# Optimization experiments

Measured on AMD Instinct MI355X. Metric: run time of the kernel, lower is better.

Reference implementation:

```python
import jax, jax.numpy as jnp
import numpy as np

NUM_HEADS_Q = 32
NUM_HEADS_KV = 8
HEAD_DIM = 128
THETA = 500000.0
B = 2
S = 1024


def _precompute_freqs(head_dim, seq_len, theta):
    half = head_dim // 2
    freqs = 1.0 / theta ** (jnp.arange(half, dtype=jnp.float32) / half)
    positions = jnp.arange(seq_len, dtype=jnp.float32)
    angles = positions[:, None] * freqs[None, :]  # (S, half)
    return jnp.cos(angles), jnp.sin(angles)


def _apply_rope(x, cos, sin):
    # x: (B, H, S, D); cos/sin: (S, D//2)
    half = x.shape[-1] // 2
    x1, x2 = x[..., :half], x[..., half:]
    c = cos[None, None]
    s = sin[None, None]
    return jnp.concatenate([x1 * c - x2 * s, x1 * s + x2 * c], axis=-1)


def setup_inputs() -> dict:
    key = jax.random.key(0)
    kq, kk, kv = jax.random.split(key, 3)
    q = jax.random.normal(kq, (B, 1, S, NUM_HEADS_Q * HEAD_DIM), dtype=jnp.float32)
    k = jax.random.normal(kk, (B, 1, S, NUM_HEADS_KV * HEAD_DIM), dtype=jnp.float32)
    v = jax.random.normal(kv, (B, 1, S, NUM_HEADS_KV * HEAD_DIM), dtype=jnp.float32)
    return {"q": q, "k": k, "v": v}


def reference(q, k, v) -> jnp.ndarray:
    D = HEAD_DIM
    gqa = NUM_HEADS_Q // NUM_HEADS_KV
    scale = 1.0 / np.sqrt(D).astype(np.float32)

    # (B,1,S,H*D) -> (B,H,S,D)
    qh = q.reshape(B, S, NUM_HEADS_Q, D).transpose(0, 2, 1, 3)
    kh = k.reshape(B, S, NUM_HEADS_KV, D).transpose(0, 2, 1, 3)
    vh = v.reshape(B, S, NUM_HEADS_KV, D).transpose(0, 2, 1, 3)

    cos, sin = _precompute_freqs(D, S, THETA)
    qh = _apply_rope(qh, cos, sin)
    kh = _apply_rope(kh, cos, sin)

    if gqa > 1:
        kh = jnp.repeat(kh, gqa, axis=1)   # (B, Hq, S, D)
        vh = jnp.repeat(vh, gqa, axis=1)

    scores = jnp.einsum('bhqd,bhkd->bhqk', qh, kh) * scale  # (B, Hq, S, S)
    causal = jnp.tril(jnp.ones((S, S), dtype=bool))
    scores = jnp.where(causal[None, None], scores, -jnp.inf)
    weights = jax.nn.softmax(scores, axis=-1)
    attn = jnp.einsum('bhqk,bhkd->bhqd', weights, vh)  # (B, Hq, S, D)
    out = attn.transpose(0, 2, 1, 3).reshape(B, 1, S, NUM_HEADS_Q * D)
    return out
```

## Files before the change

kernel.cpp:

```cpp
#include <hip/hip_runtime.h>
#include <math.h>

typedef __attribute__((ext_vector_type(4))) float f32x4;
typedef __attribute__((ext_vector_type(16))) float f32x16;
typedef __attribute__((ext_vector_type(8))) short bf16x8;

namespace {
constexpr int kB = 2;
constexpr int kS = 1024;
constexpr int kD = 128;
constexpr float kScale = 0.08838834764831845f;
constexpr float kLog2e = 1.4426950408889634f;
constexpr float kFreqC = 0.20503692777194262f;
constexpr int kKPad = 136;
constexpr int kVPad = 72;

constexpr size_t kTabOff = 0;
constexpr size_t kKOff = 512 * 1024;
constexpr size_t kVOff = kKOff + 4194304;
constexpr size_t kWsNeed = kVOff + 4194304;
}

#define VMCNT(n) asm volatile("s_waitcnt vmcnt(" #n ")" ::: "memory")

__device__ inline short f2bf(float f) {
  union { float f; unsigned u; } c{f};
  unsigned r = c.u + 0x7fffu + ((c.u >> 16) & 1u);
  return (short)(r >> 16);
}

__device__ inline unsigned pkbf(float a, float b) {
  unsigned r;
  asm("v_cvt_pk_bf16_f32 %0, %1, %2" : "=v"(r) : "v"(a), "v"(b));
  return r;
}

__device__ inline void gload16(const void* g, void* l) {
  __builtin_amdgcn_global_load_lds(
      (const __attribute__((address_space(1))) void*)g,
      (__attribute__((address_space(3))) void*)l, 16, 0, 0);
}

__global__ __launch_bounds__(256) void rope_table_k(float2* __restrict__ tab) {
  int t = blockIdx.x * 256 + threadIdx.x;
  int pos = t >> 6, j = t & 63;
  float ang = (float)pos * expf(-(float)j * kFreqC);
  float sn, cs;
  sincosf(ang, &sn, &cs);
  tab[t] = make_float2(cs, sn);
}

__global__ __launch_bounds__(256) void prep_k(
    const float* __restrict__ k, const float* __restrict__ v,
    const float2* __restrict__ tab, short* __restrict__ Kp,
    short* __restrict__ Vp) {
  __shared__ float Tl[64][68];
  int bid = blockIdx.x;
  if (bid < 1024) {
    int t2 = bid * 256 + threadIdx.x;
    int j = (t2 & 15) * 4;
    int h = (t2 >> 4) & 7;
    int s = (t2 >> 7) & 1023;
    int b = t2 >> 17;
    size_t sidx = ((size_t)b * 1024 + s) * 1024 + h * 128 + j;
    size_t didx = (((size_t)b * 8 + h) * 1024 + s) * 128 + j;
    float4 x1 = *(const float4*)&k[sidx];
    float4 x2 = *(const float4*)&k[sidx + 64];
    float4 t0 = *(const float4*)&tab[s * 64 + j];
    float4 t1 = *(const float4*)&tab[s * 64 + j + 2];
    short4 y1, y2;
    y1.x = f2bf(x1.x * t0.x - x2.x * t0.y);
    y2.x = f2bf(x1.x * t0.y + x2.x * t0.x);
    y1.y = f2bf(x1.y * t0.z - x2.y * t0.w);
    y2.y = f2bf(x1.y * t0.w + x2.y * t0.z);
    y1.z = f2bf(x1.z * t1.x - x2.z * t1.y);
    y2.z = f2bf(x1.z * t1.y + x2.z * t1.x);
    y1.w = f2bf(x1.w * t1.z - x2.w * t1.w);
    y2.w = f2bf(x1.w * t1.w + x2.w * t1.z);
    *(short4*)&Kp[didx] = y1;
    *(short4*)&Kp[didx + 64] = y2;
  } else {
    int blk = bid - 1024;
    int bh = blk >> 5;
    int rem = blk & 31;
    int s0 = (rem >> 1) * 64;
    int d0 = (rem & 1) * 64;
    int t = threadIdx.x;
#pragma unroll
    for (int i = 0; i < 4; ++i) {
      int srow = i * 16 + (t >> 4);
      int scol = (t & 15) * 4;
      float4 x = *(const float4*)&v[((size_t)(bh >> 3) * 1024 + s0 + srow) * 1024 +
                                    (bh & 7) * 128 + d0 + scol];
      *(float4*)&Tl[srow][scol] = x;
    }
    __syncthreads();
#pragma unroll
    for (int i = 0; i < 4; ++i) {
      int drow = i * 16 + (t >> 4);
      int sq = (t & 15) * 4;
      short4 y;
      y.x = f2bf(Tl[sq + 0][drow]);
      y.y = f2bf(Tl[sq + 1][drow]);
      y.z = f2bf(Tl[sq + 2][drow]);
      y.w = f2bf(Tl[sq + 3][drow]);
      *(short4*)&Vp[((size_t)bh * 128 + d0 + drow) * 1024 + s0 + sq] = y;
    }
  }
}

__global__ __launch_bounds__(256, 2) void attn32_k(
    const float* __restrict__ q, const short* __restrict__ Kp,
    const short* __restrict__ Vp, const float2* __restrict__ tab,
    float* __restrict__ out) {
  __shared__ char KV[2][32768];

  const int tid = threadIdx.x;
  const int w = tid >> 6;
  const int lane = tid & 63;
  const int l31 = lane & 31;
  const int hi5 = lane >> 5;
  const int f = ((int)blockIdx.x + (int)blockIdx.y) & 7;
  const int b = blockIdx.z;
  const int qt = b ? (7 - f) : f;
  const int hq = blockIdx.y;
  const int hkv = hq >> 2;
  const int q0 = qt * 128;
  const int nk = 2 * (qt + 1);

  const char* Kh = (const char*)(Kp + ((size_t)b * 8 + hkv) * 1024 * 128);
  const char* Vh = (const char*)(Vp + ((size_t)b * 8 + hkv) * 128 * 1024);

#define STAGE(k0_, bufi_)                                                     \
  {                                                                           \
    char* Kd = KV[bufi_];                                                     \
    char* Vd = KV[bufi_] + 16384;                                             \
    _Pragma("unroll") for (int ii = 0; ii < 4; ++ii) {                        \
      int i = w * 4 + ii;                                                     \
      int row = i * 4 + (lane >> 4);                                          \
      int srcb = ((k0_) + row) * 256 + (((lane & 15) * 16) ^ ((row & 7) << 4)); \
      gload16(Kh + srcb, Kd + i * 1024);                                      \
    }                                                                         \
    _Pragma("unroll") for (int ii = 0; ii < 4; ++ii) {                        \
      int i = w * 4 + ii;                                                     \
      int d = i * 8 + (lane >> 3);                                            \
      int srcb = d * 2048 + (k0_) * 2 + (((lane & 7) * 16) ^ ((d & 7) << 4)); \
      gload16(Vh + srcb, Vd + i * 1024);                                      \
    }                                                                         \
  }

  STAGE(0, 0);

  const int qrow = q0 + w * 32 + l31;
  const float* qp = q + ((size_t)b * 1024 + qrow) * 4096 + hq * 128;
  const float2* tp = tab + (size_t)qrow * 64;
  bf16x8 qB[8];
#pragma unroll
  for (int g = 0; g < 4; ++g) {
    int jb = g * 16 + hi5 * 8;
    float4 x1a = *(const float4*)&qp[jb];
    float4 x1b = *(const float4*)&qp[jb + 4];
    float4 x2a = *(const float4*)&qp[jb + 64];
    float4 x2b = *(const float4*)&qp[jb + 68];
    float4 t0 = *(const float4*)&tp[jb];
    float4 t1 = *(const float4*)&tp[jb + 2];
    float4 t2 = *(const float4*)&tp[jb + 4];
    float4 t3 = *(const float4*)&tp[jb + 6];
    float lo[8], hb[8];
    lo[0] = (x1a.x * t0.x - x2a.x * t0.y) * kScale;
    hb[0] = (x1a.x * t0.y + x2a.x * t0.x) * kScale;
    lo[1] = (x1a.y * t0.z - x2a.y * t0.w) * kScale;
    hb[1] = (x1a.y * t0.w + x2a.y * t0.z) * kScale;
    lo[2] = (x1a.z * t1.x - x2a.z * t1.y) * kScale;
    hb[2] = (x1a.z * t1.y + x2a.z * t1.x) * kScale;
    lo[3] = (x1a.w * t1.z - x2a.w * t1.w) * kScale;
    hb[3] = (x1a.w * t1.w + x2a.w * t1.z) * kScale;
    lo[4] = (x1b.x * t2.x - x2b.x * t2.y) * kScale;
    hb[4] = (x1b.x * t2.y + x2b.x * t2.x) * kScale;
    lo[5] = (x1b.y * t2.z - x2b.y * t2.w) * kScale;
    hb[5] = (x1b.y * t2.w + x2b.y * t2.z) * kScale;
    lo[6] = (x1b.z * t3.x - x2b.z * t3.y) * kScale;
    hb[6] = (x1b.z * t3.y + x2b.z * t3.x) * kScale;
    lo[7] = (x1b.w * t3.z - x2b.w * t3.w) * kScale;
    hb[7] = (x1b.w * t3.w + x2b.w * t3.z) * kScale;
    union { unsigned u[4]; bf16x8 v; } A, C;
#pragma unroll
    for (int ww = 0; ww < 4; ++ww) {
      A.u[ww] = pkbf(lo[2 * ww], lo[2 * ww + 1]);
      C.u[ww] = pkbf(hb[2 * ww], hb[2 * ww + 1]);
    }
    qB[g] = A.v;
    qB[g + 4] = C.v;
  }

  float m = -3e38f, l = 0.f;
  f32x16 acc[4];
#pragma unroll
  for (int dt = 0; dt < 4; ++dt)
#pragma unroll
    for (int e = 0; e < 16; ++e) acc[dt][e] = 0.f;

  int buf = 0;
  for (int t = 0; t < nk; ++t) {
    if (t < nk - 1) {
      STAGE((t + 1) * 64, buf ^ 1);
      VMCNT(8);
    } else {
      VMCNT(0);
    }
    __builtin_amdgcn_sched_barrier(0);
    __builtin_amdgcn_s_barrier();
    __builtin_amdgcn_sched_barrier(0);

    const char* Ks = KV[buf];
    const char* Vt = KV[buf] + 16384;

    f32x16 sc0, sc1;
#pragma unroll
    for (int e = 0; e < 16; ++e) { sc0[e] = 0.f; sc1[e] = 0.f; }
    const int kswz = (l31 & 7) << 4;
    __builtin_amdgcn_s_setprio(1);
#pragma unroll
    for (int c = 0; c < 8; ++c) {
      int off = c * 32 + hi5 * 16;
      bf16x8 k0f = *(const bf16x8*)(Ks + l31 * 256 + (off ^ kswz));
      bf16x8 k1f = *(const bf16x8*)(Ks + (32 + l31) * 256 + (off ^ kswz));
      sc0 = __builtin_amdgcn_mfma_f32_32x32x16_bf16(k0f, qB[c], sc0, 0, 0, 0);
      sc1 = __builtin_amdgcn_mfma_f32_32x32x16_bf16(k1f, qB[c], sc1, 0, 0, 0);
    }
    __builtin_amdgcn_s_setprio(0);

    if (64 * (t + 1) > q0 + 32 * w) {
      int kb = t * 64 + hi5 * 4;
#pragma unroll
      for (int r = 0; r < 16; ++r) {
        int off = (r & 3) + 8 * (r >> 2);
        if (kb + off > qrow) sc0[r] = -3e38f;
        if (kb + 32 + off > qrow) sc1[r] = -3e38f;
      }
    }

    float tv = -3e38f;
#pragma unroll
    for (int r = 0; r < 16; ++r) tv = fmaxf(tv, fmaxf(sc0[r], sc1[r]));
    tv = fmaxf(tv, __shfl_xor(tv, 32));
    if (!__all(tv <= m + 8.f)) {
      float mn = fmaxf(m, tv);
      float al = exp2f((m - mn) * kLog2e);
      m = mn;
      l *= al;
#pragma unroll
      for (int r = 0; r < 16; ++r) {
        float alr = __shfl(al, (r & 3) + 8 * (r >> 2) + 4 * hi5);
        acc[0][r] *= alr;
        acc[1][r] *= alr;
        acc[2][r] *= alr;
        acc[3][r] *= alr;
      }
    }
    float rs = 0.f;
#pragma unroll
    for (int r = 0; r < 16; ++r) {
      sc0[r] = exp2f((sc0[r] - m) * kLog2e);
      sc1[r] = exp2f((sc1[r] - m) * kLog2e);
      rs += sc0[r] + sc1[r];
    }
    rs += __shfl_xor(rs, 32);
    l += rs;

    __builtin_amdgcn_s_setprio(1);
#define PV_CHUNK(S, CI)                                                       \
    {                                                                         \
      unsigned p0 = pkbf(S[8 * ((CI) & 1) + 0], S[8 * ((CI) & 1) + 1]);       \
      unsigned p1 = pkbf(S[8 * ((CI) & 1) + 2], S[8 * ((CI) & 1) + 3]);       \
      unsigned p2 = pkbf(S[8 * ((CI) & 1) + 4], S[8 * ((CI) & 1) + 5]);       \
      unsigned p3 = pkbf(S[8 * ((CI) & 1) + 6], S[8 * ((CI) & 1) + 7]);       \
      asm("v_permlane32_swap_b32 %0, %1" : "+v"(p0), "+v"(p2));               \
      asm("v_permlane32_swap_b32 %0, %1" : "+v"(p1), "+v"(p3));               \
      union { unsigned u[4]; bf16x8 v; } pa;                                  \
      pa.u[0] = p0; pa.u[1] = p1; pa.u[2] = p2; pa.u[3] = p3;                 \
      int ko = (CI) * 32 + hi5 * 16;                                          \
      _Pragma("unroll") for (int dt = 0; dt < 4; ++dt) {                      \
        int d = dt * 32 + l31;                                                \
        bf16x8 vf = *(const bf16x8*)(Vt + d * 128 + (ko ^ ((d & 7) << 4)));   \
        acc[dt] =                                                             \
            __builtin_amdgcn_mfma_f32_32x32x16_bf16(pa.v, vf, acc[dt], 0, 0, 0); \
      }                                                                       \
    }
    PV_CHUNK(sc0, 0)
    PV_CHUNK(sc0, 1)
    PV_CHUNK(sc1, 2)
    PV_CHUNK(sc1, 3)
#undef PV_CHUNK
    __builtin_amdgcn_s_setprio(0);

    __builtin_amdgcn_sched_barrier(0);
    __builtin_amdgcn_s_barrier();
    __builtin_amdgcn_sched_barrier(0);
    buf ^= 1;
  }

  float linv = 1.f / l;
  const size_t obase = ((size_t)b * 1024 + q0 + w * 32) * 4096 + (size_t)hq * 128;
#pragma unroll
  for (int r = 0; r < 16; ++r) {
    int rq = (r & 3) + 8 * (r >> 2) + 4 * hi5;
    float ilr = __shfl(linv, rq);
    float* orow = out + obase + (size_t)rq * 4096 + l31;
    orow[0]  = acc[0][r] * ilr;
    orow[32] = acc[1][r] * ilr;
    orow[64] = acc[2][r] * ilr;
    orow[96] = acc[3][r] * ilr;
  }
#undef STAGE
}

template <bool USE_TAB>
__global__ __launch_bounds__(256) void attn_k(
    const float* __restrict__ q, const float* __restrict__ k,
    const float* __restrict__ v, const float2* __restrict__ tab,
    float* __restrict__ out) {
  __shared__ short Ksf[64][kKPad];
  __shared__ short Vtf[kD][kVPad];
  __shared__ short Qbuf[64 * kKPad];
  const int tid = threadIdx.x;
  const int w = tid >> 6;
  const int lane = tid & 63;
  const int lrow = lane & 15;
  const int lk8 = (lane >> 4) * 8;
  const int qt = (int)gridDim.x - 1 - (int)blockIdx.x;
  const int hq = blockIdx.y;
  const int b = blockIdx.z;
  const int hkv = hq >> 2;
  const int q0 = qt * 64;
  const float* qb = q + (size_t)b * kS * 4096 + hq * kD;
  const float* kb = k + (size_t)b * kS * 1024 + hkv * kD;
  const float* vb = v + (size_t)b * kS * 1024 + hkv * kD;
#pragma unroll
  for (int it = 0; it < 16; ++it) {
    int pi = tid + it * 256;
    int row = pi >> 6, j = pi & 63;
    int pos = q0 + row;
    float x1 = qb[(size_t)pos * 4096 + j];
    float x2 = qb[(size_t)pos * 4096 + j + 64];
    float c, s;
    if (USE_TAB) { float2 t2 = tab[(pos << 6) + j]; c = t2.x; s = t2.y; }
    else { float ang = (float)pos * __expf(-(float)j * kFreqC); __sincosf(ang, &s, &c); }
    Qbuf[row * kKPad + j]      = f2bf((x1 * c - x2 * s) * kScale);
    Qbuf[row * kKPad + j + 64] = f2bf((x1 * s + x2 * c) * kScale);
  }
  __syncthreads();
  bf16x8 qf[4];
#pragma unroll
  for (int d = 0; d < 4; ++d)
    qf[d] = *(const bf16x8*)&Qbuf[(w * 16 + lrow) * kKPad + d * 32 + lk8];
  __syncthreads();
  short* myP = Qbuf + w * 16 * kVPad;
  float mS[4] = {-3e38f, -3e38f, -3e38f, -3e38f};
  float lS[4] = {0.f, 0.f, 0.f, 0.f};
  f32x4 acc[8];
#pragma unroll
  for (int dt = 0; dt < 8; ++dt) acc[dt] = f32x4{0.f, 0.f, 0.f, 0.f};
  for (int kt = 0; kt <= qt; ++kt) {
    const int k0 = kt * 64;
#pragma unroll
    for (int it = 0; it < 16; ++it) {
      int pi = tid + it * 256;
      int row = pi >> 6, j = pi & 63;
      int pos = k0 + row;
      float x1 = kb[(size_t)pos * 1024 + j];
      float x2 = kb[(size_t)pos * 1024 + j + 64];
      float c, s;
      if (USE_TAB) { float2 t2 = tab[(pos << 6) + j]; c = t2.x; s = t2.y; }
      else { float ang = (float)pos * __expf(-(float)j * kFreqC); __sincosf(ang, &s, &c); }
      Ksf[row][j]      = f2bf(x1 * c - x2 * s);
      Ksf[row][j + 64] = f2bf(x1 * s + x2 * c);
    }
#pragma unroll
    for (int it = 0; it < 8; ++it) {
      int f = (tid + it * 256) * 4;
      int row = f >> 7, col = f & 127;
      const float4 v4 = *(const float4*)(vb + (size_t)(k0 + row) * 1024 + col);
      Vtf[col + 0][row] = f2bf(v4.x);
      Vtf[col + 1][row] = f2bf(v4.y);
      Vtf[col + 2][row] = f2bf(v4.z);
      Vtf[col + 3][row] = f2bf(v4.w);
    }
    __syncthreads();
    f32x4 sc[4];
#pragma unroll
    for (int ct = 0; ct < 4; ++ct) {
      sc[ct] = f32x4{0.f, 0.f, 0.f, 0.f};
#pragma unroll
      for (int d = 0; d < 4; ++d) {
        bf16x8 kf = *(const bf16x8*)&Ksf[ct * 16 + lrow][d * 32 + lk8];
        sc[ct] = __builtin_amdgcn_mfma_f32_16x16x32_bf16(qf[d], kf, sc[ct], 0, 0, 0);
      }
    }
    if (kt == qt) {
#pragma unroll
      for (int ct = 0; ct < 4; ++ct) {
        int col = ct * 16 + lrow;
#pragma unroll
        for (int r = 0; r < 4; ++r) {
          int row = w * 16 + (lane >> 4) * 4 + r;
          if (col > row) sc[ct][r] = -3e38f;
        }
      }
    }
#pragma unroll
    for (int r = 0; r < 4; ++r) {
      float t = fmaxf(fmaxf(sc[0][r], sc[1][r]), fmaxf(sc[2][r], sc[3][r]));
      t = fmaxf(t, __shfl_xor(t, 1));
      t = fmaxf(t, __shfl_xor(t, 2));
      t = fmaxf(t, __shfl_xor(t, 4));
      t = fmaxf(t, __shfl_xor(t, 8));
      float mn = fmaxf(mS[r], t);
      float al = exp2f((mS[r] - mn) * kLog2e);
      float rs = 0.f;
#pragma unroll
      for (int ct = 0; ct < 4; ++ct) {
        float p = exp2f((sc[ct][r] - mn) * kLog2e);
        sc[ct][r] = p;
        rs += p;
      }
      rs += __shfl_xor(rs, 1);
      rs += __shfl_xor(rs, 2);
      rs += __shfl_xor(rs, 4);
      rs += __shfl_xor(rs, 8);
      lS[r] = lS[r] * al + rs;
      mS[r] = mn;
#pragma unroll
      for (int dt = 0; dt < 8; ++dt) acc[dt][r] *= al;
    }
#pragma unroll
    for (int ct = 0; ct < 4; ++ct)
#pragma unroll
      for (int r = 0; r < 4; ++r)
        myP[((lane >> 4) * 4 + r) * kVPad + ct * 16 + lrow] = f2bf(sc[ct][r]);
#pragma unroll
    for (int ks = 0; ks < 2; ++ks) {
      bf16x8 pf = *(const bf16x8*)&myP[lrow * kVPad + ks * 32 + lk8];
#pragma unroll
      for (int dt = 0; dt < 8; ++dt) {
        bf16x8 vf = *(const bf16x8*)&Vtf[dt * 16 + lrow][ks * 32 + lk8];
        acc[dt] = __builtin_amdgcn_mfma_f32_16x16x32_bf16(pf, vf, acc[dt], 0, 0, 0);
      }
    }
    __syncthreads();
  }
  float il[4];
#pragma unroll
  for (int r = 0; r < 4; ++r) il[r] = 1.f / lS[r];
  float* ob = out + ((size_t)b * kS + q0 + w * 16) * 4096 + hq * kD;
#pragma unroll
  for (int dt = 0; dt < 8; ++dt)
#pragma unroll
    for (int r = 0; r < 4; ++r)
      ob[((lane >> 4) * 4 + r) * 4096 + dt * 16 + lrow] = acc[dt][r] * il[r];
}

extern "C" void kernel_launch(void* const* d_in, const int* in_sizes, int n_in,
                              void* d_out, int out_size, void* d_ws, size_t ws_size,
                              hipStream_t stream) {
  const float* q = (const float*)d_in[0];
  const float* k = (const float*)d_in[1];
  const float* v = (const float*)d_in[2];
  float* out = (float*)d_out;

  if (ws_size >= kWsNeed) {
    float2* tab = (float2*)((char*)d_ws + kTabOff);
    short* Kp = (short*)((char*)d_ws + kKOff);
    short* Vp = (short*)((char*)d_ws + kVOff);
    rope_table_k<<<256, 256, 0, stream>>>(tab);
    prep_k<<<1536, 256, 0, stream>>>(k, v, tab, Kp, Vp);
    dim3 grid(8, 32, kB);
    attn32_k<<<grid, 256, 0, stream>>>(q, Kp, Vp, tab, out);
  } else if (ws_size >= 512 * 1024) {
    float2* tab = (float2*)d_ws;
    rope_table_k<<<256, 256, 0, stream>>>(tab);
    dim3 grid(16, 32, kB);
    attn_k<true><<<grid, 256, 0, stream>>>(q, k, v, tab, out);
  } else {
    dim3 grid(16, 32, kB);
    attn_k<false><<<grid, 256, 0, stream>>>(q, k, v, nullptr, out);
  }
}
```

Measured before the change: 64.15 us.

## Fuse rope table into prep kernel and triple-buffer 32-key tiles with per-wave causal skip

The separate rope-table kernel is folded into the prep launch: K blocks compute sin/cos inline and extra blocks write the table used by the Q path. This removes one launch and the dependency between the two kernels. The attention kernel now streams 32-key K/V tiles through a three-buffer LDS ring, prefetching two tiles ahead, where before it double-buffered 64-key tiles. Each wave skips the tiles that lie wholly above its causal diagonal and masks only its diagonal tile. The old query-tile/batch remapping is dropped for a simple reversed order, and the Q loads are issued before the first stages so their latency overlaps them. In exchange, there are more loop iterations and barriers, and the K path repeats transcendental work per element.

Result: slower. 72.09 us (+12.4%).

```diff
diff --git a/kernel.cpp b/kernel.cpp
--- a/kernel.cpp
+++ b/kernel.cpp
@@ -52,8 +52,7 @@
 
 __global__ __launch_bounds__(256) void prep_k(
     const float* __restrict__ k, const float* __restrict__ v,
-    const float2* __restrict__ tab, short* __restrict__ Kp,
-    short* __restrict__ Vp) {
+    short* __restrict__ Kp, short* __restrict__ Vp, float2* __restrict__ tab) {
   __shared__ float Tl[64][68];
   int bid = blockIdx.x;
   if (bid < 1024) {
@@ -66,20 +65,24 @@
     size_t didx = (((size_t)b * 8 + h) * 1024 + s) * 128 + j;
     float4 x1 = *(const float4*)&k[sidx];
     float4 x2 = *(const float4*)&k[sidx + 64];
-    float4 t0 = *(const float4*)&tab[s * 64 + j];
-    float4 t1 = *(const float4*)&tab[s * 64 + j + 2];
+    float cs[4], sn[4];
+#pragma unroll
+    for (int jj = 0; jj < 4; ++jj) {
+      float ang = (float)s * expf(-(float)(j + jj) * kFreqC);
+      sincosf(ang, &sn[jj], &cs[jj]);
+    }
     short4 y1, y2;
-    y1.x = f2bf(x1.x * t0.x - x2.x * t0.y);
-    y2.x = f2bf(x1.x * t0.y + x2.x * t0.x);
-    y1.y = f2bf(x1.y * t0.z - x2.y * t0.w);
-    y2.y = f2bf(x1.y * t0.w + x2.y * t0.z);
-    y1.z = f2bf(x1.z * t1.x - x2.z * t1.y);
-    y2.z = f2bf(x1.z * t1.y + x2.z * t1.x);
-    y1.w = f2bf(x1.w * t1.z - x2.w * t1.w);
-    y2.w = f2bf(x1.w * t1.w + x2.w * t1.z);
+    y1.x = f2bf(x1.x * cs[0] - x2.x * sn[0]);
+    y2.x = f2bf(x1.x * sn[0] + x2.x * cs[0]);
+    y1.y = f2bf(x1.y * cs[1] - x2.y * sn[1]);
+    y2.y = f2bf(x1.y * sn[1] + x2.y * cs[1]);
+    y1.z = f2bf(x1.z * cs[2] - x2.z * sn[2]);
+    y2.z = f2bf(x1.z * sn[2] + x2.z * cs[2]);
+    y1.w = f2bf(x1.w * cs[3] - x2.w * sn[3]);
+    y2.w = f2bf(x1.w * sn[3] + x2.w * cs[3]);
     *(short4*)&Kp[didx] = y1;
     *(short4*)&Kp[didx + 64] = y2;
-  } else {
+  } else if (bid < 1536) {
     int blk = bid - 1024;
     int bh = blk >> 5;
     int rem = blk & 31;
@@ -106,66 +109,83 @@
       y.w = f2bf(Tl[sq + 3][drow]);
       *(short4*)&Vp[((size_t)bh * 128 + d0 + drow) * 1024 + s0 + sq] = y;
     }
-  }
-}
-
-__global__ __launch_bounds__(256, 2) void attn32_k(
+  } else {
+    int t = (bid - 1536) * 256 + threadIdx.x;
+    int pos = t >> 6, j = t & 63;
+    float ang = (float)pos * expf(-(float)j * kFreqC);
+    float sn, cs;
+    sincosf(ang, &sn, &cs);
+    tab[t] = make_float2(cs, sn);
+  }
+}
+
+__global__ __launch_bounds__(256, 2) void attn32b_k(
     const float* __restrict__ q, const short* __restrict__ Kp,
     const short* __restrict__ Vp, const float2* __restrict__ tab,
     float* __restrict__ out) {
-  __shared__ char KV[2][32768];
+  __shared__ char KV[3][16384];
 
   const int tid = threadIdx.x;
   const int w = tid >> 6;
   const int lane = tid & 63;
   const int l31 = lane & 31;
   const int hi5 = lane >> 5;
-  const int f = ((int)blockIdx.x + (int)blockIdx.y) & 7;
+  const int qt = 7 - (int)blockIdx.x;
+  const int hq = blockIdx.y;
   const int b = blockIdx.z;
-  const int qt = b ? (7 - f) : f;
-  const int hq = blockIdx.y;
   const int hkv = hq >> 2;
   const int q0 = qt * 128;
-  const int nk = 2 * (qt + 1);
+  const int nk = 4 * (qt + 1);
+  const int qg = q0 + w * 32 + l31;
+  const int tmask = 4 * qt + w;
 
   const char* Kh = (const char*)(Kp + ((size_t)b * 8 + hkv) * 1024 * 128);
   const char* Vh = (const char*)(Vp + ((size_t)b * 8 + hkv) * 128 * 1024);
 
-#define STAGE(k0_, bufi_)                                                     \
+#define STAGE32B(k0_, dst_)                                                   \
   {                                                                           \
-    char* Kd = KV[bufi_];                                                     \
-    char* Vd = KV[bufi_] + 16384;                                             \
-    _Pragma("unroll") for (int ii = 0; ii < 4; ++ii) {                        \
-      int i = w * 4 + ii;                                                     \
+    char* Kd = (char*)(dst_);                                                 \
+    char* Vd = (char*)(dst_) + 8192;                                          \
+    _Pragma("unroll") for (int ii = 0; ii < 2; ++ii) {                        \
+      int i = w * 2 + ii;                                                     \
       int row = i * 4 + (lane >> 4);                                          \
       int srcb = ((k0_) + row) * 256 + (((lane & 15) * 16) ^ ((row & 7) << 4)); \
       gload16(Kh + srcb, Kd + i * 1024);                                      \
     }                                                                         \
-    _Pragma("unroll") for (int ii = 0; ii < 4; ++ii) {                        \
-      int i = w * 4 + ii;                                                     \
-      int d = i * 8 + (lane >> 3);                                            \
-      int srcb = d * 2048 + (k0_) * 2 + (((lane & 7) * 16) ^ ((d & 7) << 4)); \
+    _Pragma("unroll") for (int ii = 0; ii < 2; ++ii) {                        \
+      int i = w * 2 + ii;                                                     \
+      int d = i * 16 + (lane >> 2);                                           \
+      int srcb = d * 2048 + (k0_) * 2 + (((lane & 3) * 16) ^ ((d & 3) << 4)); \
       gload16(Vh + srcb, Vd + i * 1024);                                      \
     }                                                                         \
   }
 
-  STAGE(0, 0);
-
-  const int qrow = q0 + w * 32 + l31;
-  const float* qp = q + ((size_t)b * 1024 + qrow) * 4096 + hq * 128;
-  const float2* tp = tab + (size_t)qrow * 64;
-  bf16x8 qB[8];
+  const float* qp = q + ((size_t)b * 1024 + qg) * 4096 + hq * 128;
+  const float2* tp = tab + (size_t)qg * 64;
+  float4 x1v[8], x2v[8], tv4[16];
 #pragma unroll
   for (int g = 0; g < 4; ++g) {
     int jb = g * 16 + hi5 * 8;
-    float4 x1a = *(const float4*)&qp[jb];
-    float4 x1b = *(const float4*)&qp[jb + 4];
-    float4 x2a = *(const float4*)&qp[jb + 64];
-    float4 x2b = *(const float4*)&qp[jb + 68];
-    float4 t0 = *(const float4*)&tp[jb];
-    float4 t1 = *(const float4*)&tp[jb + 2];
-    float4 t2 = *(const float4*)&tp[jb + 4];
-    float4 t3 = *(const float4*)&tp[jb + 6];
+    x1v[2 * g] = *(const float4*)&qp[jb];
+    x1v[2 * g + 1] = *(const float4*)&qp[jb + 4];
+    x2v[2 * g] = *(const float4*)&qp[jb + 64];
+    x2v[2 * g + 1] = *(const float4*)&qp[jb + 68];
+    tv4[4 * g + 0] = *(const float4*)&tp[jb];
+    tv4[4 * g + 1] = *(const float4*)&tp[jb + 2];
+    tv4[4 * g + 2] = *(const float4*)&tp[jb + 4];
+    tv4[4 * g + 3] = *(const float4*)&tp[jb + 6];
+  }
+
+  STAGE32B(0, KV[0]);
+  STAGE32B(32, KV[1]);
+
+  bf16x8 qB[8];
+#pragma unroll
+  for (int g = 0; g < 4; ++g) {
+    float4 x1a = x1v[2 * g], x1b = x1v[2 * g + 1];
+    float4 x2a = x2v[2 * g], x2b = x2v[2 * g + 1];
+    float4 t0 = tv4[4 * g], t1 = tv4[4 * g + 1], t2 = tv4[4 * g + 2],
+           t3 = tv4[4 * g + 3];
     float lo[8], hb[8];
     lo[0] = (x1a.x * t0.x - x2a.x * t0.y) * kScale;
     hb[0] = (x1a.x * t0.y + x2a.x * t0.x) * kScale;
@@ -200,11 +220,15 @@
 #pragma unroll
     for (int e = 0; e < 16; ++e) acc[dt][e] = 0.f;
 
-  int buf = 0;
+  int bc = 0;
   for (int t = 0; t < nk; ++t) {
-    if (t < nk - 1) {
-      STAGE((t + 1) * 64, buf ^ 1);
+    if (t + 2 < nk) {
+      int bs = bc + 2;
+      if (bs >= 3) bs -= 3;
+      STAGE32B((t + 2) * 32, KV[bs]);
       VMCNT(8);
+    } else if (t + 1 < nk) {
+      VMCNT(4);
     } else {
       VMCNT(0);
     }
@@ -212,92 +236,87 @@
     __builtin_amdgcn_s_barrier();
     __builtin_amdgcn_sched_barrier(0);
 
-    const char* Ks = KV[buf];
-    const char* Vt = KV[buf] + 16384;
-
-    f32x16 sc0, sc1;
-#pragma unroll
-    for (int e = 0; e < 16; ++e) { sc0[e] = 0.f; sc1[e] = 0.f; }
-    const int kswz = (l31 & 7) << 4;
-    __builtin_amdgcn_s_setprio(1);
-#pragma unroll
-    for (int c = 0; c < 8; ++c) {
-      int off = c * 32 + hi5 * 16;
-      bf16x8 k0f = *(const bf16x8*)(Ks + l31 * 256 + (off ^ kswz));
-      bf16x8 k1f = *(const bf16x8*)(Ks + (32 + l31) * 256 + (off ^ kswz));
-      sc0 = __builtin_amdgcn_mfma_f32_32x32x16_bf16(k0f, qB[c], sc0, 0, 0, 0);
-      sc1 = __builtin_amdgcn_mfma_f32_32x32x16_bf16(k1f, qB[c], sc1, 0, 0, 0);
-    }
-    __builtin_amdgcn_s_setprio(0);
-
-    if (64 * (t + 1) > q0 + 32 * w) {
-      int kb = t * 64 + hi5 * 4;
+    if (t <= tmask) {
+      const char* Ks = KV[bc];
+      const char* Vt = KV[bc] + 8192;
+
+      f32x16 sc;
+#pragma unroll
+      for (int e = 0; e < 16; ++e) sc[e] = 0.f;
+      const int kswz = (l31 & 7) << 4;
+      __builtin_amdgcn_s_setprio(1);
+#pragma unroll
+      for (int c = 0; c < 8; ++c) {
+        bf16x8 kf = *(const bf16x8*)(Ks + l31 * 256 +
+                                     ((c * 32 + hi5 * 16) ^ kswz));
+        sc = __builtin_amdgcn_mfma_f32_32x32x16_bf16(kf, qB[c], sc, 0, 0, 0);
+      }
+      __builtin_amdgcn_s_setprio(0);
+
+      if (t == tmask) {
+#pragma unroll
+        for (int r = 0; r < 16; ++r) {
+          int key = t * 32 + (r & 3) + 8 * (r >> 2) + 4 * hi5;
+          if (key > qg) sc[r] = -3e38f;
+        }
+      }
+
+      float tv = -3e38f;
+#pragma unroll
+      for (int r = 0; r < 16; ++r) tv = fmaxf(tv, sc[r]);
+      tv = fmaxf(tv, __shfl_xor(tv, 32));
+      if (!__all(tv <= m + 8.f)) {
+        float mn = fmaxf(m, tv);
+        float al = exp2f((m - mn) * kLog2e);
+        m = mn;
+        l *= al;
+#pragma unroll
+        for (int r = 0; r < 16; ++r) {
+          float alr = __shfl(al, (r & 3) + 8 * (r >> 2) + 4 * hi5);
+          acc[0][r] *= alr;
+          acc[1][r] *= alr;
+          acc[2][r] *= alr;
+          acc[3][r] *= alr;
+        }
+      }
+      float rs = 0.f;
 #pragma unroll
       for (int r = 0; r < 16; ++r) {
-        int off = (r & 3) + 8 * (r >> 2);
-        if (kb + off > qrow) sc0[r] = -3e38f;
-        if (kb + 32 + off > qrow) sc1[r] = -3e38f;
-      }
-    }
-
-    float tv = -3e38f;
-#pragma unroll
-    for (int r = 0; r < 16; ++r) tv = fmaxf(tv, fmaxf(sc0[r], sc1[r]));
-    tv = fmaxf(tv, __shfl_xor(tv, 32));
-    if (!__all(tv <= m + 8.f)) {
-      float mn = fmaxf(m, tv);
-      float al = exp2f((m - mn) * kLog2e);
-      m = mn;
-      l *= al;
-#pragma unroll
-      for (int r = 0; r < 16; ++r) {
-        float alr = __shfl(al, (r & 3) + 8 * (r >> 2) + 4 * hi5);
-        acc[0][r] *= alr;
-        acc[1][r] *= alr;
-        acc[2][r] *= alr;
-        acc[3][r] *= alr;
-      }
-    }
-    float rs = 0.f;
-#pragma unroll
-    for (int r = 0; r < 16; ++r) {
-      sc0[r] = exp2f((sc0[r] - m) * kLog2e);
-      sc1[r] = exp2f((sc1[r] - m) * kLog2e);
-      rs += sc0[r] + sc1[r];
-    }
-    rs += __shfl_xor(rs, 32);
-    l += rs;
-
-    __builtin_amdgcn_s_setprio(1);
-#define PV_CHUNK(S, CI)                                                       \
-    {                                                                         \
-      unsigned p0 = pkbf(S[8 * ((CI) & 1) + 0], S[8 * ((CI) & 1) + 1]);       \
-      unsigned p1 = pkbf(S[8 * ((CI) & 1) + 2], S[8 * ((CI) & 1) + 3]);       \
-      unsigned p2 = pkbf(S[8 * ((CI) & 1) + 4], S[8 * ((CI) & 1) + 5]);       \
-      unsigned p3 = pkbf(S[8 * ((CI) & 1) + 6], S[8 * ((CI) & 1) + 7]);       \
-      asm("v_permlane32_swap_b32 %0, %1" : "+v"(p0), "+v"(p2));               \
-      asm("v_permlane32_swap_b32 %0, %1" : "+v"(p1), "+v"(p3));               \
-      union { unsigned u[4]; bf16x8 v; } pa;                                  \
-      pa.u[0] = p0; pa.u[1] = p1; pa.u[2] = p2; pa.u[3] = p3;                 \
-      int ko = (CI) * 32 + hi5 * 16;                                          \
-      _Pragma("unroll") for (int dt = 0; dt < 4; ++dt) {                      \
-        int d = dt * 32 + l31;                                                \
-        bf16x8 vf = *(const bf16x8*)(Vt + d * 128 + (ko ^ ((d & 7) << 4)));   \
-        acc[dt] =                                                             \
-            __builtin_amdgcn_mfma_f32_32x32x16_bf16(pa.v, vf, acc[dt], 0, 0, 0); \
-      }                                                                       \
-    }
-    PV_CHUNK(sc0, 0)
-    PV_CHUNK(sc0, 1)
-    PV_CHUNK(sc1, 2)
-    PV_CHUNK(sc1, 3)
+        sc[r] = exp2f((sc[r] - m) * kLog2e);
+        rs += sc[r];
+      }
+      rs += __shfl_xor(rs, 32);
+      l += rs;
+
+      __builtin_amdgcn_s_setprio(1);
+#define PV_CHUNK(CI)                                                          \
+      {                                                                       \
+        unsigned p0 = pkbf(sc[8 * (CI) + 0], sc[8 * (CI) + 1]);               \
+        unsigned p1 = pkbf(sc[8 * (CI) + 2], sc[8 * (CI) + 3]);               \
+        unsigned p2 = pkbf(sc[8 * (CI) + 4], sc[8 * (CI) + 5]);               \
+        unsigned p3 = pkbf(sc[8 * (CI) + 6], sc[8 * (CI) + 7]);               \
+        asm("v_permlane32_swap_b32 %0, %1" : "+v"(p0), "+v"(p2));             \
+        asm("v_permlane32_swap_b32 %0, %1" : "+v"(p1), "+v"(p3));             \
+        union { unsigned u[4]; bf16x8 v; } pa;                                \
+        pa.u[0] = p0; pa.u[1] = p1; pa.u[2] = p2; pa.u[3] = p3;               \
+        int ko = (CI) * 32 + hi5 * 16;                                        \
+        _Pragma("unroll") for (int dt = 0; dt < 4; ++dt) {                    \
+          int d = dt * 32 + l31;                                              \
+          bf16x8 vf = *(const bf16x8*)(Vt + d * 64 + (ko ^ ((d & 3) << 4)));  \
+          acc[dt] = __builtin_amdgcn_mfma_f32_32x32x16_bf16(pa.v, vf,         \
+                                                            acc[dt], 0, 0, 0); \
+        }                                                                     \
+      }
+      PV_CHUNK(0)
+      PV_CHUNK(1)
 #undef PV_CHUNK
-    __builtin_amdgcn_s_setprio(0);
+      __builtin_amdgcn_s_setprio(0);
+    }
 
     __builtin_amdgcn_sched_barrier(0);
     __builtin_amdgcn_s_barrier();
     __builtin_amdgcn_sched_barrier(0);
-    buf ^= 1;
+    bc = (bc == 2) ? 0 : bc + 1;
   }
 
   float linv = 1.f / l;
@@ -312,7 +331,7 @@
     orow[64] = acc[2][r] * ilr;
     orow[96] = acc[3][r] * ilr;
   }
-#undef STAGE
+#undef STAGE32B
 }
 
 template <bool USE_TAB>
@@ -472,10 +491,9 @@
     float2* tab = (float2*)((char*)d_ws + kTabOff);
     short* Kp = (short*)((char*)d_ws + kKOff);
     short* Vp = (short*)((char*)d_ws + kVOff);
-    rope_table_k<<<256, 256, 0, stream>>>(tab);
-    prep_k<<<1536, 256, 0, stream>>>(k, v, tab, Kp, Vp);
+    prep_k<<<1792, 256, 0, stream>>>(k, v, Kp, Vp, tab);
     dim3 grid(8, 32, kB);
-    attn32_k<<<grid, 256, 0, stream>>>(q, Kp, Vp, tab, out);
+    attn32b_k<<<grid, 256, 0, stream>>>(q, Kp, Vp, tab, out);
   } else if (ws_size >= 512 * 1024) {
     float2* tab = (float2*)d_ws;
     rope_table_k<<<256, 256, 0, stream>>>(tab);
```
